# Performance work log

Measured on AMD Instinct MI355X. Metric: run time of the kernel, lower is better.

## Reference

```python
import jax, jax.numpy as jnp
import numpy as np

E = 30000
NUM_BASIS = 10
CUTOFF = 4.0
HIDDEN = 16
WNUM = 9216  # 64*64 + 64*32 + 32*32 + 32*64
INV_S3 = 1.0 / np.sqrt(3.0)
PW0 = np.sqrt(1.0 / 96.0)  # component/element norm, out 0e (alpha=1, x=64+32)
PW1 = np.sqrt(3.0 / 96.0)  # out 1o (alpha=3, x=64+32)


def setup_inputs() -> dict:
    key = jax.random.key(0)
    ks = jax.random.split(key, 8)
    x = jax.random.normal(ks[0], (E, 160), jnp.float32)
    rel_pos_sh = jax.random.normal(ks[1], (E, 4), jnp.float32)
    # distances strictly inside (0, cutoff) so envelope 1/d is finite
    distance = (jax.random.uniform(ks[2], (E, 1), jnp.float32) * 0.99 + 0.005) * CUTOFF
    # Bessel frequencies: n*pi, n=1..num_basis (trainable param in PyG)
    freq = jnp.arange(1, NUM_BASIS + 1, dtype=jnp.float32) * jnp.pi
    lim1 = 1.0 / np.sqrt(NUM_BASIS)
    w1 = jax.random.uniform(ks[3], (NUM_BASIS, HIDDEN), jnp.float32, -lim1, lim1)
    b1 = jax.random.uniform(ks[4], (HIDDEN,), jnp.float32, -lim1, lim1)
    lim2 = 1.0 / np.sqrt(HIDDEN)
    w2 = jax.random.uniform(ks[5], (HIDDEN, WNUM), jnp.float32, -lim2, lim2)
    b2 = jax.random.uniform(ks[6], (WNUM,), jnp.float32, -lim2, lim2)
    return dict(x=x, rel_pos_sh=rel_pos_sh, distance=distance,
                freq=freq, w1=w1, b1=b1, w2=w2, b2=b2)


def _radial_weights(distance, freq, w1, b1, w2, b2):
    d = distance[:, 0] / CUTOFF  # [E]
    d5 = d ** 5
    env = (1.0 / d - 28.0 * d5 + 48.0 * d5 * d - 21.0 * d5 * d * d) * (d < 1.0).astype(d.dtype)
    basis = env[:, None] * jnp.sin(freq[None, :] * d[:, None])  # [E, num_basis]
    h = jax.nn.silu(basis @ w1 + b1)
    return h @ w2 + b2  # [E, 9216]


def _tp(x, rel_pos_sh, weights):
    # split per-edge weights into the 4 CG paths (e3nn instruction order)
    Wa = weights[:, 0:4096].reshape(E, 64, 64)      # (0e,0e)->0e
    Wb = weights[:, 4096:6144].reshape(E, 64, 32)   # (0e,1o)->1o
    Wc = weights[:, 6144:7168].reshape(E, 32, 32)   # (1o,0e)->1o
    Wd = weights[:, 7168:9216].reshape(E, 32, 64)   # (1o,1o)->0e
    x0 = x[:, :64]                     # [E,64]   64x0e
    x1 = x[:, 64:].reshape(E, 32, 3)   # [E,32,3] 32x1o
    sh0 = rel_pos_sh[:, 0]             # [E]
    sh1 = rel_pos_sh[:, 1:4]           # [E,3]
    out0 = PW0 * (jnp.einsum('euw,eu->ew', Wa, x0) * sh0[:, None]
                  + INV_S3 * jnp.einsum('euw,eum,em->ew', Wd, x1, sh1))
    out1 = PW1 * INV_S3 * (jnp.einsum('euw,eu,em->ewm', Wb, x0, sh1)
                           + jnp.einsum('euw,eum->ewm', Wc, x1) * sh0[:, None, None])
    return jnp.concatenate([out0, out1.reshape(E, 96)], axis=-1)  # [E,160]


def reference(x, rel_pos_sh, distance, freq, w1, b1, w2, b2):
    weights = _radial_weights(distance, freq, w1, b1, w2, b2)
    return _tp(x, rel_pos_sh, weights)
```

## Files before the change

kernel.cpp:

```cpp
#include <hip/hip_runtime.h>
#include <hip/hip_bf16.h>
#include <cstddef>

#define E_TOTAL 30000
#define INV_S3 0.57735026918962576f
#define PW0    0.10206207261596575f
#define PW1    0.17677669529663687f

typedef __attribute__((ext_vector_type(8))) short bf16x8;
typedef __attribute__((ext_vector_type(4))) float f32x4;

#define NA_SH (34*6*512)
#define NB_SH (17*4*512)
#define NC_SH (17*2*512)
#define NH_BLKS 118

__device__ __forceinline__ short f2bf(float v) {
    union { __hip_bfloat16 h; short s; } u;
    u.h = __float2bfloat16(v);
    return u.s;
}
__device__ __forceinline__ f32x4 ld4(const float* p) {
    return *reinterpret_cast<const f32x4*>(p);
}

__global__ void prep_all(const float* __restrict__ dist, const float* __restrict__ freq,
                         const float* __restrict__ w1, const float* __restrict__ b1,
                         const float* __restrict__ w2, const float* __restrict__ b2,
                         float* __restrict__ h_out,
                         short* __restrict__ Ba, short* __restrict__ Bb, short* __restrict__ Bc)
{
    const float C1 = PW1 * INV_S3, C2 = PW0 * INV_S3;
    const int t = threadIdx.x;
    if (blockIdx.x < NH_BLKS) {
        int e = blockIdx.x * 256 + t;
        if (e >= E_TOTAL) return;
        float d  = dist[e] * 0.25f;
        float d2 = d * d, d5 = d2 * d2 * d;
        float env = 1.0f / d - 28.0f * d5 + 48.0f * d5 * d - 21.0f * d5 * d * d;
        env = (d < 1.0f) ? env : 0.0f;
        float basis[10];
#pragma unroll
        for (int k = 0; k < 10; ++k) basis[k] = env * sinf(freq[k] * d);
#pragma unroll
        for (int j = 0; j < 16; ++j) {
            float a = b1[j];
#pragma unroll
            for (int k = 0; k < 10; ++k) a = fmaf(basis[k], w1[k * 16 + j], a);
            h_out[(size_t)e * 16 + j] = a / (1.0f + __expf(-a));
        }
        return;
    }
    __shared__ float sw[3072];
    int blk = blockIdx.x - NH_BLKS;
    if (blk < 34) {
        int c = blk;
        int cc = (c < 17) ? c : c - 17;
        int ubase = (c < 17) ? 0 : 32;
        const float* src = (cc < 16) ? (w2 + (size_t)cc * 9216) : b2;
        const float4* pA = reinterpret_cast<const float4*>(src + ubase * 64);
        for (int i = t; i < 512; i += 256) reinterpret_cast<float4*>(sw)[i] = pA[i];
        const float4* pB = reinterpret_cast<const float4*>(src + 4096 + ubase * 32);
        if (t < 256) reinterpret_cast<float4*>(sw + 2048)[t] = pB[t];
        __syncthreads();
        for (int i = t; i < 384; i += 256) {
            int nt = i >> 6, lane = i & 63, kg = lane >> 4, jc = lane & 15;
            int w = nt * 16 + jc;
            bf16x8 fr;
#pragma unroll
            for (int b = 0; b < 8; ++b) {
                int u = kg * 8 + b;
                float v = (w < 64) ? PW0 * sw[u * 64 + w]
                                   : C1  * sw[2048 + u * 32 + (w - 64)];
                fr[b] = f2bf(v);
            }
            *reinterpret_cast<bf16x8*>(Ba + ((size_t)(c * 6 + nt)) * 512 + lane * 8) = fr;
        }
    } else if (blk < 51) {
        int c = blk - 34;
        const float* src = (c < 16) ? (w2 + (size_t)c * 9216) : b2;
        const float4* p = reinterpret_cast<const float4*>(src + 7168);
        for (int i = t; i < 512; i += 256) reinterpret_cast<float4*>(sw)[i] = p[i];
        __syncthreads();
        {
            int nt = t >> 6, lane = t & 63, kg = lane >> 4, jc = lane & 15;
            int w = nt * 16 + jc;
            bf16x8 fr;
#pragma unroll
            for (int b = 0; b < 8; ++b) { int u = kg * 8 + b; fr[b] = f2bf(C2 * sw[u * 64 + w]); }
            *reinterpret_cast<bf16x8*>(Bb + ((size_t)(c * 4 + nt)) * 512 + lane * 8) = fr;
        }
    } else {
        int c = blk - 51;
        const float* src = (c < 16) ? (w2 + (size_t)c * 9216) : b2;
        const float4* p = reinterpret_cast<const float4*>(src + 6144);
        if (t < 256) reinterpret_cast<float4*>(sw)[t] = p[t];
        __syncthreads();
        if (t < 128) {
            int nt = t >> 6, lane = t & 63, kg = lane >> 4, jc = lane & 15;
            int w = nt * 16 + jc;
            bf16x8 fr;
#pragma unroll
            for (int b = 0; b < 8; ++b) { int u = kg * 8 + b; fr[b] = f2bf(C1 * sw[u * 32 + w]); }
            *reinterpret_cast<bf16x8*>(Bc + ((size_t)(c * 2 + nt)) * 512 + lane * 8) = fr;
        }
    }
}

__device__ __forceinline__ void mstep6(const bf16x8* __restrict__ Bp, int base, float hc,
                                       const float (&xs)[8], int lane, f32x4 (&acc)[6]) {
    bf16x8 af;
#pragma unroll
    for (int b = 0; b < 8; ++b) af[b] = f2bf(hc * xs[b]);
#pragma unroll
    for (int nt = 0; nt < 6; ++nt) {
        bf16x8 bc = Bp[(size_t)(base + nt) * 64 + lane];
        acc[nt] = __builtin_amdgcn_mfma_f32_16x16x32_bf16(af, bc, acc[nt], 0, 0, 0);
    }
}
__device__ __forceinline__ void mstep4(const bf16x8* __restrict__ Bp, int base, float hc,
                                       const float (&xs)[8], int lane, f32x4 (&acc)[4]) {
    bf16x8 af;
#pragma unroll
    for (int b = 0; b < 8; ++b) af[b] = f2bf(hc * xs[b]);
#pragma unroll
    for (int nt = 0; nt < 4; ++nt) {
        bf16x8 bc = Bp[(size_t)(base + nt) * 64 + lane];
        acc[nt] = __builtin_amdgcn_mfma_f32_16x16x32_bf16(af, bc, acc[nt], 0, 0, 0);
    }
}
__device__ __forceinline__ void gstep(const bf16x8* __restrict__ Bp, int base, float coef,
                                      const float (&x1w)[24], int lane, f32x4 (&acc)[3][2]) {
    bf16x8 am[3];
#pragma unroll
    for (int m = 0; m < 3; ++m)
#pragma unroll
        for (int b = 0; b < 8; ++b) am[m][b] = f2bf(coef * x1w[3 * b + m]);
#pragma unroll
    for (int nt = 0; nt < 2; ++nt) {
        bf16x8 bc = Bp[(size_t)(base + nt) * 64 + lane];
#pragma unroll
        for (int m = 0; m < 3; ++m)
            acc[m][nt] = __builtin_amdgcn_mfma_f32_16x16x32_bf16(am[m], bc, acc[m][nt], 0, 0, 0);
    }
}

__launch_bounds__(256, 3)
__global__ void conv_main(const float* __restrict__ x, const float* __restrict__ rp,
                          const float* __restrict__ h_arr,
                          const short* __restrict__ Ba, const short* __restrict__ Bb,
                          const short* __restrict__ Bc, float* __restrict__ out)
{
    __shared__ float ssh[64][4];
    const int t = threadIdx.x, lane = t & 63, wave = t >> 6;
    const int kg = lane >> 4, jc = lane & 15;
    const int e0 = blockIdx.x * 64;

    { int ee = t >> 2, c4 = t & 3;
      ssh[ee][c4] = (e0 + ee < E_TOTAL) ? rp[(size_t)(e0 + ee) * 4 + c4] : 0.f; }

    const int erow = wave * 16 + jc;
    const size_t eA = (size_t)(e0 + erow);
    const bool ev = (e0 + erow) < E_TOTAL;
    const float* xp = x + eA * 160;
    const float* hp = h_arr + eA * 16;

    float h[16];
#pragma unroll
    for (int i = 0; i < 4; ++i) {
        f32x4 q = ev ? ld4(hp + 4 * i) : f32x4{0.f, 0.f, 0.f, 0.f};
        h[4*i] = q[0]; h[4*i+1] = q[1]; h[4*i+2] = q[2]; h[4*i+3] = q[3];
    }
    float x0lo[8], x0hi[8];
#pragma unroll
    for (int i = 0; i < 2; ++i) {
        f32x4 q = ev ? ld4(xp + kg * 8 + 4 * i) : f32x4{0.f, 0.f, 0.f, 0.f};
        x0lo[4*i] = q[0]; x0lo[4*i+1] = q[1]; x0lo[4*i+2] = q[2]; x0lo[4*i+3] = q[3];
        f32x4 r = ev ? ld4(xp + 32 + kg * 8 + 4 * i) : f32x4{0.f, 0.f, 0.f, 0.f};
        x0hi[4*i] = r[0]; x0hi[4*i+1] = r[1]; x0hi[4*i+2] = r[2]; x0hi[4*i+3] = r[3];
    }
    float x1w[24];
#pragma unroll
    for (int i = 0; i < 6; ++i) {
        f32x4 q = ev ? ld4(xp + 64 + 24 * kg + 4 * i) : f32x4{0.f, 0.f, 0.f, 0.f};
        x1w[4*i] = q[0]; x1w[4*i+1] = q[1]; x1w[4*i+2] = q[2]; x1w[4*i+3] = q[3];
    }
    __syncthreads();

    const float sh0 = ssh[erow][0];
    float z[8];
    { float s1 = ssh[erow][1], s2 = ssh[erow][2], s3 = ssh[erow][3];
#pragma unroll
      for (int u = 0; u < 8; ++u)
          z[u] = x1w[3*u] * s1 + x1w[3*u+1] * s2 + x1w[3*u+2] * s3; }

    const bf16x8* BpA = reinterpret_cast<const bf16x8*>(Ba);
    const bf16x8* BpB = reinterpret_cast<const bf16x8*>(Bb);
    const bf16x8* BpC = reinterpret_cast<const bf16x8*>(Bc);

    f32x4 accA[6] = {};
#pragma unroll
    for (int c = 0; c < 16; ++c) mstep6(BpA, c * 6, h[c], x0lo, lane, accA);
    mstep6(BpA, 16 * 6, 1.0f, x0lo, lane, accA);
#pragma unroll
    for (int c = 0; c < 16; ++c) mstep6(BpA, (17 + c) * 6, h[c], x0hi, lane, accA);
    mstep6(BpA, 33 * 6, 1.0f, x0hi, lane, accA);

    f32x4 accB[4] = {};
#pragma unroll
    for (int c = 0; c < 16; ++c) mstep4(BpB, c * 4, h[c], z, lane, accB);
    mstep4(BpB, 16 * 4, 1.0f, z, lane, accB);

#pragma unroll
    for (int nt = 0; nt < 4; ++nt)
#pragma unroll
        for (int r = 0; r < 4; ++r) {
            int row = wave * 16 + 4 * kg + r;
            if (e0 + row < E_TOTAL)
                out[(size_t)(e0 + row) * 160 + nt * 16 + jc] =
                    ssh[row][0] * accA[nt][r] + accB[nt][r];
        }

    f32x4 accG[3][2] = {};
#pragma unroll
    for (int c = 0; c < 16; ++c) gstep(BpC, c * 2, sh0 * h[c], x1w, lane, accG);
    gstep(BpC, 16 * 2, sh0, x1w, lane, accG);

#pragma unroll
    for (int m = 0; m < 3; ++m)
#pragma unroll
        for (int nt = 0; nt < 2; ++nt)
#pragma unroll
            for (int r = 0; r < 4; ++r) {
                int row = wave * 16 + 4 * kg + r;
                int w = nt * 16 + jc;
                if (e0 + row < E_TOTAL)
                    out[(size_t)(e0 + row) * 160 + 64 + w * 3 + m] =
                        accA[4 + nt][r] * ssh[row][1 + m] + accG[m][nt][r];
            }
}

extern "C" void kernel_launch(void* const* d_in, const int* in_sizes, int n_in,
                              void* d_out, int out_size, void* d_ws, size_t ws_size,
                              hipStream_t stream) {
    const float* x    = (const float*)d_in[0];
    const float* rp   = (const float*)d_in[1];
    const float* dist = (const float*)d_in[2];
    const float* freq = (const float*)d_in[3];
    const float* w1   = (const float*)d_in[4];
    const float* b1   = (const float*)d_in[5];
    const float* w2   = (const float*)d_in[6];
    const float* b2   = (const float*)d_in[7];
    float* out = (float*)d_out;

    float* h_arr = (float*)d_ws;
    short* Ba = (short*)((char*)d_ws + 1920000);
    short* Bb = Ba + NA_SH;
    short* Bc = Bb + NB_SH;

    prep_all<<<NH_BLKS + 68, 256, 0, stream>>>(dist, freq, w1, b1, w2, b2,
                                               h_arr, Ba, Bb, Bc);
    conv_main<<<(E_TOTAL + 63) / 64, 256, 0, stream>>>(x, rp, h_arr, Ba, Bb, Bc, out);
}
```

Baseline: 128.3 us.

## Stage B weight fragments into LDS with double-buffered global_load_lds pipeline

Instead of every wave loading the bf16 B fragments from global memory, the block cooperatively copies them into LDS with async global_load_lds. The Ba/Bb chunks use a double-buffered pipeline, and all of Bc is preloaded. The A, B and Bb paths are fused into one 17-chunk loop with a barrier per chunk. This trades occupancy (launch bound lowered to 2 blocks per CU, about 68 KB of LDS) and adds barriers, in exchange for less redundant global/L2 traffic.

```diff
diff --git a/kernel.cpp b/kernel.cpp
--- a/kernel.cpp
+++ b/kernel.cpp
@@ -23,6 +23,10 @@
 __device__ __forceinline__ f32x4 ld4(const float* p) {
     return *reinterpret_cast<const f32x4*>(p);
 }
+
+#define GL16(gp, lp) __builtin_amdgcn_global_load_lds( \
+    (const __attribute__((address_space(1))) void*)(gp), \
+    (__attribute__((address_space(3))) void*)(lp), 16, 0, 0)
 
 __global__ void prep_all(const float* __restrict__ dist, const float* __restrict__ freq,
                          const float* __restrict__ w1, const float* __restrict__ b1,
@@ -107,63 +111,48 @@
     }
 }
 
-__device__ __forceinline__ void mstep6(const bf16x8* __restrict__ Bp, int base, float hc,
-                                       const float (&xs)[8], int lane, f32x4 (&acc)[6]) {
-    bf16x8 af;
-#pragma unroll
-    for (int b = 0; b < 8; ++b) af[b] = f2bf(hc * xs[b]);
-#pragma unroll
-    for (int nt = 0; nt < 6; ++nt) {
-        bf16x8 bc = Bp[(size_t)(base + nt) * 64 + lane];
-        acc[nt] = __builtin_amdgcn_mfma_f32_16x16x32_bf16(af, bc, acc[nt], 0, 0, 0);
-    }
-}
-__device__ __forceinline__ void mstep4(const bf16x8* __restrict__ Bp, int base, float hc,
-                                       const float (&xs)[8], int lane, f32x4 (&acc)[4]) {
-    bf16x8 af;
-#pragma unroll
-    for (int b = 0; b < 8; ++b) af[b] = f2bf(hc * xs[b]);
-#pragma unroll
-    for (int nt = 0; nt < 4; ++nt) {
-        bf16x8 bc = Bp[(size_t)(base + nt) * 64 + lane];
-        acc[nt] = __builtin_amdgcn_mfma_f32_16x16x32_bf16(af, bc, acc[nt], 0, 0, 0);
-    }
-}
-__device__ __forceinline__ void gstep(const bf16x8* __restrict__ Bp, int base, float coef,
-                                      const float (&x1w)[24], int lane, f32x4 (&acc)[3][2]) {
-    bf16x8 am[3];
-#pragma unroll
-    for (int m = 0; m < 3; ++m)
-#pragma unroll
-        for (int b = 0; b < 8; ++b) am[m][b] = f2bf(coef * x1w[3 * b + m]);
-#pragma unroll
-    for (int nt = 0; nt < 2; ++nt) {
-        bf16x8 bc = Bp[(size_t)(base + nt) * 64 + lane];
-#pragma unroll
-        for (int m = 0; m < 3; ++m)
-            acc[m][nt] = __builtin_amdgcn_mfma_f32_16x16x32_bf16(am[m], bc, acc[m][nt], 0, 0, 0);
-    }
-}
-
-__launch_bounds__(256, 3)
+__device__ __forceinline__ void stage_chunk(const short* __restrict__ Ba,
+                                            const short* __restrict__ Bb,
+                                            short* dst, int c, int t) {
+    const short* slo = Ba + c * 3072;
+    const short* shi = Ba + (17 + c) * 3072;
+    const short* sbt = Bb + c * 2048;
+    GL16(slo + t * 8,            dst + t * 8);
+    if (t < 128) GL16(slo + (t + 256) * 8, dst + (t + 256) * 8);
+    GL16(shi + t * 8,            dst + 3072 + t * 8);
+    if (t < 128) GL16(shi + (t + 256) * 8, dst + 3072 + (t + 256) * 8);
+    GL16(sbt + t * 8,            dst + 6144 + t * 8);
+}
+
+__launch_bounds__(256, 2)
 __global__ void conv_main(const float* __restrict__ x, const float* __restrict__ rp,
                           const float* __restrict__ h_arr,
                           const short* __restrict__ Ba, const short* __restrict__ Bb,
                           const short* __restrict__ Bc, float* __restrict__ out)
 {
-    __shared__ float ssh[64][4];
+    __shared__ __align__(16) char smem[68608];
+    short* sgam = reinterpret_cast<short*>(smem);
+    short* sstg = reinterpret_cast<short*>(smem + 34816);
+    float (*ssh)[4] = reinterpret_cast<float(*)[4]>(smem + 67584);
+
     const int t = threadIdx.x, lane = t & 63, wave = t >> 6;
     const int kg = lane >> 4, jc = lane & 15;
     const int e0 = blockIdx.x * 64;
 
+#pragma unroll
+    for (int k2 = 0; k2 < 8; ++k2)
+        GL16(Bc + (t + k2 * 256) * 8, sgam + (t + k2 * 256) * 8);
+    if (t < 128) GL16(Bc + (t + 2048) * 8, sgam + (t + 2048) * 8);
+    stage_chunk(Ba, Bb, sstg, 0, t);
+
     { int ee = t >> 2, c4 = t & 3;
       ssh[ee][c4] = (e0 + ee < E_TOTAL) ? rp[(size_t)(e0 + ee) * 4 + c4] : 0.f; }
 
     const int erow = wave * 16 + jc;
-    const size_t eA = (size_t)(e0 + erow);
+    const size_t eAi = (size_t)(e0 + erow);
     const bool ev = (e0 + erow) < E_TOTAL;
-    const float* xp = x + eA * 160;
-    const float* hp = h_arr + eA * 16;
+    const float* xp = x + eAi * 160;
+    const float* hp = h_arr + eAi * 16;
 
     float h[16];
 #pragma unroll
@@ -194,22 +183,46 @@
       for (int u = 0; u < 8; ++u)
           z[u] = x1w[3*u] * s1 + x1w[3*u+1] * s2 + x1w[3*u+2] * s3; }
 
-    const bf16x8* BpA = reinterpret_cast<const bf16x8*>(Ba);
-    const bf16x8* BpB = reinterpret_cast<const bf16x8*>(Bb);
-    const bf16x8* BpC = reinterpret_cast<const bf16x8*>(Bc);
-
     f32x4 accA[6] = {};
-#pragma unroll
-    for (int c = 0; c < 16; ++c) mstep6(BpA, c * 6, h[c], x0lo, lane, accA);
-    mstep6(BpA, 16 * 6, 1.0f, x0lo, lane, accA);
-#pragma unroll
-    for (int c = 0; c < 16; ++c) mstep6(BpA, (17 + c) * 6, h[c], x0hi, lane, accA);
-    mstep6(BpA, 33 * 6, 1.0f, x0hi, lane, accA);
-
     f32x4 accB[4] = {};
-#pragma unroll
-    for (int c = 0; c < 16; ++c) mstep4(BpB, c * 4, h[c], z, lane, accB);
-    mstep4(BpB, 16 * 4, 1.0f, z, lane, accB);
+    f32x4 accG[3][2] = {};
+
+    int cur = 0;
+#pragma unroll
+    for (int c = 0; c < 17; ++c) {
+        short* buf = sstg + cur * 8192;
+        if (c < 16) stage_chunk(Ba, Bb, sstg + (cur ^ 1) * 8192, c + 1, t);
+
+        const float hc = (c < 16) ? h[c] : 1.0f;
+        bf16x8 blo[6], bhi[6], bbt[4];
+#pragma unroll
+        for (int nt = 0; nt < 6; ++nt) {
+            blo[nt] = *reinterpret_cast<const bf16x8*>(buf + nt * 512 + lane * 8);
+            bhi[nt] = *reinterpret_cast<const bf16x8*>(buf + 3072 + nt * 512 + lane * 8);
+        }
+#pragma unroll
+        for (int nt = 0; nt < 4; ++nt)
+            bbt[nt] = *reinterpret_cast<const bf16x8*>(buf + 6144 + nt * 512 + lane * 8);
+
+        bf16x8 aflo, afhi, afz;
+#pragma unroll
+        for (int b = 0; b < 8; ++b) {
+            aflo[b] = f2bf(hc * x0lo[b]);
+            afhi[b] = f2bf(hc * x0hi[b]);
+            afz[b]  = f2bf(hc * z[b]);
+        }
+#pragma unroll
+        for (int nt = 0; nt < 6; ++nt) {
+            accA[nt] = __builtin_amdgcn_mfma_f32_16x16x32_bf16(aflo, blo[nt], accA[nt], 0, 0, 0);
+            accA[nt] = __builtin_amdgcn_mfma_f32_16x16x32_bf16(afhi, bhi[nt], accA[nt], 0, 0, 0);
+        }
+#pragma unroll
+        for (int nt = 0; nt < 4; ++nt)
+            accB[nt] = __builtin_amdgcn_mfma_f32_16x16x32_bf16(afz, bbt[nt], accB[nt], 0, 0, 0);
+
+        __syncthreads();
+        cur ^= 1;
+    }
 
 #pragma unroll
     for (int nt = 0; nt < 4; ++nt)
@@ -221,10 +234,24 @@
                     ssh[row][0] * accA[nt][r] + accB[nt][r];
         }
 
-    f32x4 accG[3][2] = {};
-#pragma unroll
-    for (int c = 0; c < 16; ++c) gstep(BpC, c * 2, sh0 * h[c], x1w, lane, accG);
-    gstep(BpC, 16 * 2, sh0, x1w, lane, accG);
+#pragma unroll
+    for (int c = 0; c < 17; ++c) {
+        const float coef = (c < 16) ? sh0 * h[c] : sh0;
+        bf16x8 bg[2];
+#pragma unroll
+        for (int nt = 0; nt < 2; ++nt)
+            bg[nt] = *reinterpret_cast<const bf16x8*>(sgam + (c * 2 + nt) * 512 + lane * 8);
+        bf16x8 am[3];
+#pragma unroll
+        for (int m = 0; m < 3; ++m)
+#pragma unroll
+            for (int b = 0; b < 8; ++b) am[m][b] = f2bf(coef * x1w[3 * b + m]);
+#pragma unroll
+        for (int nt = 0; nt < 2; ++nt)
+#pragma unroll
+            for (int m = 0; m < 3; ++m)
+                accG[m][nt] = __builtin_amdgcn_mfma_f32_16x16x32_bf16(am[m], bg[nt], accG[m][nt], 0, 0, 0);
+    }
 
 #pragma unroll
     for (int m = 0; m < 3; ++m)
```

Result: faster. 105.4 us (-17.9%).
